# Kernel tuning notes

Measured on AMD Instinct MI355X. Metric: run time of the kernel, lower is better.

The kernel has to match this reference:

```python
import jax, jax.numpy as jnp
import numpy as np

BIG = jnp.float32(9e15)


def _normalize(sim, mask):
    # min/max are taken over positions where mask == 0 (faithful to the torch code)
    mn = jnp.min(jnp.where(mask == 0.0, sim, BIG), axis=-1, keepdims=True)
    mx = jnp.max(jnp.where(mask == 0.0, sim, -BIG), axis=-1, keepdims=True)
    return (sim - mn) / (mx - mn)


def setup_inputs() -> dict:
    key = jax.random.key(0)
    k1, k2 = jax.random.split(key)
    B, M = 4096, 8192
    return {
        "similarity_matrix": jax.random.normal(k1, (B, B), dtype=jnp.float32),
        "memory_bank_matrix": jax.random.normal(k2, (B, M), dtype=jnp.float32),
        "num_neighbors": 32,
        "temperature": jnp.ones((), dtype=jnp.float32),
    }


def reference(similarity_matrix, memory_bank_matrix, num_neighbors, temperature):
    sim = similarity_matrix
    B = sim.shape[0]
    eye = jnp.eye(B, dtype=sim.dtype)

    # --- neighbor masks via top-k over off-diagonal similarities ---
    sim_noself = jnp.where(eye == 0.0, sim, -BIG)
    _, topk_idx = jax.lax.top_k(sim_noself, num_neighbors)       # [B, k]
    rows = jnp.broadcast_to(jnp.arange(B)[:, None], topk_idx.shape)
    neighbor_mask = jnp.zeros((B, B), dtype=sim.dtype).at[rows, topk_idx].set(1.0)
    extended_mask = eye.at[rows, topk_idx].set(1.0)

    # --- centrality from memory bank ---
    centrality = jnp.mean(memory_bank_matrix, axis=-1)           # [B]
    cent_exp = jnp.broadcast_to(centrality[None, :], (B, B))

    norm_sim = _normalize(sim, extended_mask)
    norm_cent = _normalize(cent_exp, extended_mask)

    adjusted = jnp.where(neighbor_mask == 1.0, norm_sim - norm_cent, -BIG)

    # --- positive weights ---
    pw = jax.nn.softmax(adjusted * temperature, axis=-1)
    pw = jnp.where(neighbor_mask == 1.0, pw, 0.0)
    pw = jnp.where(eye == 1.0, 1.0, pw)  # fill_diagonal_(1.0)

    # --- masked log-softmax loss ---
    masked_sim = jnp.where(extended_mask == 1.0, sim, -BIG)
    logp = jax.nn.log_softmax(masked_sim, axis=-1) * pw
    per_row = -jnp.sum(logp, axis=-1) / jnp.sum(pw, axis=-1)
    return jnp.mean(per_row)
```

## Files before the change

### kernel.cpp

```cpp
#include <hip/hip_runtime.h>
#include <cmath>


#define CAP 256
#define MAXIT 40

__device__ inline float wave_max_f(float x) {
#pragma unroll
    for (int off = 32; off > 0; off >>= 1) x = fmaxf(x, __shfl_xor(x, off, 64));
    return x;
}
__device__ inline float wave_min_f(float x) {
#pragma unroll
    for (int off = 32; off > 0; off >>= 1) x = fminf(x, __shfl_xor(x, off, 64));
    return x;
}
__device__ inline float wave_sum_f(float x) {
#pragma unroll
    for (int off = 32; off > 0; off >>= 1) x += __shfl_xor(x, off, 64);
    return x;
}
__device__ inline unsigned int wave_min_u32(unsigned int x) {
#pragma unroll
    for (int off = 32; off > 0; off >>= 1) {
        unsigned int o = (unsigned int)__shfl_xor((int)x, off, 64);
        x = (o < x) ? o : x;
    }
    return x;
}

__device__ inline unsigned int f_to_key(float f) {
    unsigned int u = __float_as_uint(f);
    return u ^ ((u & 0x80000000u) ? 0xFFFFFFFFu : 0x80000000u);
}
__device__ inline float key_to_f(unsigned int key) {
    unsigned int u = key ^ ((key & 0x80000000u) ? 0x80000000u : 0xFFFFFFFFu);
    return __uint_as_float(u);
}

__global__ __launch_bounds__(256)
void cent_kernel(const float* __restrict__ mem, float* __restrict__ cent, int M) {
    __shared__ float s[4];
    const int row = blockIdx.x;
    const float4* p = (const float4*)(mem + (size_t)row * M);
    const int n4 = M >> 2;
    float acc = 0.0f;
    int i = threadIdx.x;
    for (; i + 1792 < n4; i += 2048) {
        float4 q0 = p[i], q1 = p[i + 256], q2 = p[i + 512], q3 = p[i + 768];
        float4 q4 = p[i + 1024], q5 = p[i + 1280], q6 = p[i + 1536], q7 = p[i + 1792];
        acc += ((q0.x + q0.y) + (q0.z + q0.w)) + ((q1.x + q1.y) + (q1.z + q1.w))
             + ((q2.x + q2.y) + (q2.z + q2.w)) + ((q3.x + q3.y) + (q3.z + q3.w))
             + ((q4.x + q4.y) + (q4.z + q4.w)) + ((q5.x + q5.y) + (q5.z + q5.w))
             + ((q6.x + q6.y) + (q6.z + q6.w)) + ((q7.x + q7.y) + (q7.z + q7.w));
    }
    for (; i < n4; i += 256) {
        float4 q = p[i];
        acc += (q.x + q.y) + (q.z + q.w);
    }
    acc = wave_sum_f(acc);
    const int lane = threadIdx.x & 63, wid = threadIdx.x >> 6;
    if (lane == 0) s[wid] = acc;
    __syncthreads();
    if (threadIdx.x == 0) cent[row] = (s[0] + s[1] + s[2] + s[3]) / (float)M;
}

__global__ __launch_bounds__(256)
void row_loss_kernel(const float* __restrict__ sim,
                     const float* __restrict__ cent,
                     const int* __restrict__ knn,
                     const float* __restrict__ temp_p,
                     float* __restrict__ per_row, int B) {
    __shared__ __align__(16) unsigned long long cand[CAP];
    __shared__ unsigned long long s_sel[64];
    __shared__ unsigned long long s_p33;
    __shared__ unsigned int s_kmin[4];
    __shared__ float s_cmin[4], s_cmax[4];
    __shared__ unsigned int s_cnt;
    __shared__ float s_diag;

    const int row = blockIdx.x, tid = threadIdx.x;
    const int lane = tid & 63, wid = tid >> 6;
    const int   k    = knn[0];
    const float temp = temp_p[0];

    unsigned int keys[16];
    unsigned int kmin = 0xFFFFFFFFu;
    const float4* rp = (const float4*)(sim + (size_t)row * B);
#pragma unroll
    for (int c = 0; c < 4; ++c) {
        float4 q = rp[c * 256 + tid];
        float t[4] = {q.x, q.y, q.z, q.w};
#pragma unroll
        for (int m = 0; m < 4; ++m) {
            const int j = c * 1024 + tid * 4 + m;
            unsigned int key = f_to_key(t[m]);
            if (j == row) { s_diag = t[m]; key = 0u; }
            else if (key < kmin) kmin = key;
            keys[c * 4 + m] = key;
        }
    }
    { unsigned int w = wave_min_u32(kmin); if (lane == 0) s_kmin[wid] = w; }
    if (tid == 0) { s_cnt = 0; s_p33 = ((unsigned long long)1u) << 32; }

    unsigned int keyT = f_to_key(2.0f), loK = 0u, hiK = 0xFFFFFFFFu, cnt = 0;
    const unsigned int need = (unsigned int)k + 1u;
    float cmin, cmax;
    const float4* cp = (const float4*)cent;
    for (int it = 0; it < MAXIT; ++it) {
        cmin = INFINITY; cmax = -INFINITY;
        __syncthreads();
#pragma unroll
        for (int c = 0; c < 4; ++c) {
            float4 q = cp[c * 256 + tid];
            float t[4] = {q.x, q.y, q.z, q.w};
#pragma unroll
            for (int m = 0; m < 4; ++m) {
                const unsigned int key = keys[c * 4 + m];
                if (key == 0u) continue;
                if (key > keyT) {
                    const unsigned int pos = atomicAdd(&s_cnt, 1u);
                    if (pos < CAP)
                        cand[pos] = ((unsigned long long)key << 32) |
                                    (unsigned long long)(0xFFFFFFFFu -
                                        (unsigned int)(c * 1024 + tid * 4 + m));
                } else {
                    cmin = fminf(cmin, t[m]);
                    cmax = fmaxf(cmax, t[m]);
                }
            }
        }
        { float a = wave_min_f(cmin), b = wave_max_f(cmax);
          if (lane == 0) { s_cmin[wid] = a; s_cmax[wid] = b; } }
        __syncthreads();
        cnt = s_cnt;
        if (cnt >= need && cnt <= CAP) break;
        if (cnt < need) { hiK = keyT; keyT = loK + ((keyT - loK) >> 1); }
        else            { loK = keyT; keyT = keyT + ((hiK - keyT) >> 1); }
        if (tid == 0) s_cnt = 0;
    }
    if (wid != 0) return;

    {
        const unsigned int n = min(cnt, (unsigned int)CAP);
        const unsigned int p0 = lane, p1 = lane + 64u, p2 = lane + 128u, p3 = lane + 192u;
        unsigned long long own0 = 0ull, own1 = 0ull, own2 = 0ull, own3 = 0ull;
        if (p0 < n) own0 = cand[p0];
        if (p1 < n) own1 = cand[p1];
        if (p2 < n) own2 = cand[p2];
        if (p3 < n) own3 = cand[p3];
        unsigned int r0 = 0, r1 = 0, r2 = 0, r3 = 0;
        const ulonglong2* c2 = (const ulonglong2*)cand;
        const unsigned int np = n >> 1;
        for (unsigned int o = 0; o < np; ++o) {
            ulonglong2 pr = c2[o];
            r0 += (pr.x > own0) ? 1u : 0u; r0 += (pr.y > own0) ? 1u : 0u;
            r1 += (pr.x > own1) ? 1u : 0u; r1 += (pr.y > own1) ? 1u : 0u;
            r2 += (pr.x > own2) ? 1u : 0u; r2 += (pr.y > own2) ? 1u : 0u;
            r3 += (pr.x > own3) ? 1u : 0u; r3 += (pr.y > own3) ? 1u : 0u;
        }
        if (n & 1u) {
            unsigned long long x = cand[n - 1u];
            r0 += (x > own0) ? 1u : 0u; r1 += (x > own1) ? 1u : 0u;
            r2 += (x > own2) ? 1u : 0u; r3 += (x > own3) ? 1u : 0u;
        }
        float cmin2 = INFINITY, cmax2 = -INFINITY;
        const unsigned int uk = (unsigned int)k;
#define HANDLE(P, OWN, R)                                                     \
        if ((P) < n) {                                                        \
            if ((R) < uk) s_sel[R] = (OWN);                                   \
            else if ((R) == uk) s_p33 = (OWN);                                \
            if ((R) >= uk) {                                                  \
                const int jj = (int)(0xFFFFFFFFu - (unsigned int)(OWN));      \
                const float cv = cent[jj];                                    \
                cmin2 = fminf(cmin2, cv);                                     \
                cmax2 = fmaxf(cmax2, cv);                                     \
            }                                                                 \
        }
        HANDLE(p0, own0, r0)
        HANDLE(p1, own1, r1)
        HANDLE(p2, own2, r2)
        HANDLE(p3, own3, r3)
#undef HANDLE
        __builtin_amdgcn_wave_barrier();
        cmin2 = wave_min_f(cmin2);
        cmax2 = wave_max_f(cmax2);
        const float mn_c = fminf(cmin2,
            fminf(fminf(s_cmin[0], s_cmin[1]), fminf(s_cmin[2], s_cmin[3])));
        const float mx_c = fmaxf(cmax2,
            fmaxf(fmaxf(s_cmax[0], s_cmax[1]), fmaxf(s_cmax[2], s_cmax[3])));
        const unsigned int kminb =
            min(min(s_kmin[0], s_kmin[1]), min(s_kmin[2], s_kmin[3]));
        const float mn_s = key_to_f(kminb);
        const float mx_s = key_to_f((unsigned int)(s_p33 >> 32));

        const float sdiag = s_diag;
        const bool  act = (lane < k);
        const unsigned long long sel = act ? s_sel[lane] : 0ull;
        const float sj = act ? key_to_f((unsigned int)(sel >> 32)) : -INFINITY;
        const int   j  = act ? (int)(0xFFFFFFFFu - (unsigned int)sel) : 0;
        const float cj = cent[j];

        float a = -INFINITY;
        if (act) {
            const float ns = (sj - mn_s) / (mx_s - mn_s);
            const float nc = (cj - mn_c) / (mx_c - mn_c);
            a = (ns - nc) * temp;
        }
        const float am   = wave_max_f(a);
        const float e    = act ? expf(a - am) : 0.0f;
        const float esum = wave_sum_f(e);
        const float pw   = e / esum;

        const float m2  = fmaxf(wave_max_f(sj), sdiag);
        const float ex  = act ? expf(sj - m2) : 0.0f;
        const float lse = m2 + logf(wave_sum_f(ex) + expf(sdiag - m2));

        const float num = wave_sum_f(act ? pw * (sj - lse) : 0.0f) + (sdiag - lse);
        const float den = 1.0f + wave_sum_f(pw);
        if (lane == 0) per_row[row] = -num / den;
    }
}

__global__ __launch_bounds__(256)
void reduce_kernel(const float* __restrict__ per_row, float* __restrict__ out, int B) {
    __shared__ float s[4];
    float acc = 0.0f;
    const float4* p = (const float4*)per_row;
    const int n4 = B >> 2;
    for (int i = threadIdx.x; i < n4; i += 256) {
        float4 q = p[i];
        acc += (q.x + q.y) + (q.z + q.w);
    }
    acc = wave_sum_f(acc);
    const int lane = threadIdx.x & 63, wid = threadIdx.x >> 6;
    if (lane == 0) s[wid] = acc;
    __syncthreads();
    if (threadIdx.x == 0) out[0] = (s[0] + s[1] + s[2] + s[3]) / (float)B;
}

extern "C" void kernel_launch(void* const* d_in, const int* in_sizes, int n_in,
                              void* d_out, int out_size, void* d_ws, size_t ws_size,
                              hipStream_t stream) {
    const float* sim  = (const float*)d_in[0];
    const float* mem  = (const float*)d_in[1];
    const int*   knn  = (const int*)d_in[2];
    const float* temp = (const float*)d_in[3];
    float* out     = (float*)d_out;
    float* cent    = (float*)d_ws;
    float* per_row = (float*)d_ws + 4096;

    const int B = (int)(std::sqrt((double)in_sizes[0]) + 0.5);
    const int M = in_sizes[1] / B;

    cent_kernel<<<B, 256, 0, stream>>>(mem, cent, M);
    row_loss_kernel<<<B, 256, 0, stream>>>(sim, cent, knn, temp, per_row, B);
    reduce_kernel<<<1, 256, 0, stream>>>(per_row, out, B);
}
```

Baseline: 56.31 us.

## Merge centrality and top-k selection into one launch, defer centrality min/max to finale

Centrality averaging and per-row top-k threshold search now run in one interleaved grid, so the memory-bank read and the similarity read overlap instead of running back to back. The centrality min/max over non-neighbour columns no longer sits inside the bisection loop. It moves to a new finale kernel that builds a per-row bitmask of neighbours and scans the centrality vector once. The final mean is folded into the finale through a last-block atomic counter. The costs are workspace round-trips for the selected candidates and headers, plus reliance on the counter being reset in pass 1.

```diff
diff --git a/kernel.cpp b/kernel.cpp
--- a/kernel.cpp
+++ b/kernel.cpp
@@ -39,50 +39,52 @@
 }
 
 __global__ __launch_bounds__(256)
-void cent_kernel(const float* __restrict__ mem, float* __restrict__ cent, int M) {
-    __shared__ float s[4];
-    const int row = blockIdx.x;
-    const float4* p = (const float4*)(mem + (size_t)row * M);
-    const int n4 = M >> 2;
-    float acc = 0.0f;
-    int i = threadIdx.x;
-    for (; i + 1792 < n4; i += 2048) {
-        float4 q0 = p[i], q1 = p[i + 256], q2 = p[i + 512], q3 = p[i + 768];
-        float4 q4 = p[i + 1024], q5 = p[i + 1280], q6 = p[i + 1536], q7 = p[i + 1792];
-        acc += ((q0.x + q0.y) + (q0.z + q0.w)) + ((q1.x + q1.y) + (q1.z + q1.w))
-             + ((q2.x + q2.y) + (q2.z + q2.w)) + ((q3.x + q3.y) + (q3.z + q3.w))
-             + ((q4.x + q4.y) + (q4.z + q4.w)) + ((q5.x + q5.y) + (q5.z + q5.w))
-             + ((q6.x + q6.y) + (q6.z + q6.w)) + ((q7.x + q7.y) + (q7.z + q7.w));
-    }
-    for (; i < n4; i += 256) {
-        float4 q = p[i];
-        acc += (q.x + q.y) + (q.z + q.w);
-    }
-    acc = wave_sum_f(acc);
-    const int lane = threadIdx.x & 63, wid = threadIdx.x >> 6;
-    if (lane == 0) s[wid] = acc;
-    __syncthreads();
-    if (threadIdx.x == 0) cent[row] = (s[0] + s[1] + s[2] + s[3]) / (float)M;
-}
-
-__global__ __launch_bounds__(256)
-void row_loss_kernel(const float* __restrict__ sim,
-                     const float* __restrict__ cent,
-                     const int* __restrict__ knn,
-                     const float* __restrict__ temp_p,
-                     float* __restrict__ per_row, int B) {
+void pass1_kernel(const float* __restrict__ sim,
+                  const float* __restrict__ mem,
+                  const int* __restrict__ knn,
+                  float* __restrict__ cent,
+                  uint4* __restrict__ hdr,
+                  unsigned long long* __restrict__ selbuf,
+                  unsigned int* __restrict__ ctr,
+                  int B, int M) {
     __shared__ __align__(16) unsigned long long cand[CAP];
-    __shared__ unsigned long long s_sel[64];
     __shared__ unsigned long long s_p33;
     __shared__ unsigned int s_kmin[4];
-    __shared__ float s_cmin[4], s_cmax[4];
     __shared__ unsigned int s_cnt;
     __shared__ float s_diag;
-
-    const int row = blockIdx.x, tid = threadIdx.x;
+    __shared__ float s_red[4];
+
+    const int bid = blockIdx.x, tid = threadIdx.x;
     const int lane = tid & 63, wid = tid >> 6;
-    const int   k    = knn[0];
-    const float temp = temp_p[0];
+    const int g = bid >> 3;
+    const int row = (g >> 1) * 8 + (bid & 7);
+
+    if ((g & 1) == 0) {
+        if (bid == 0 && tid == 0) ctr[0] = 0u;
+        const float4* p = (const float4*)(mem + (size_t)row * M);
+        const int n4 = M >> 2;
+        float acc = 0.0f;
+        int i = tid;
+        for (; i + 1792 < n4; i += 2048) {
+            float4 q0 = p[i], q1 = p[i + 256], q2 = p[i + 512], q3 = p[i + 768];
+            float4 q4 = p[i + 1024], q5 = p[i + 1280], q6 = p[i + 1536], q7 = p[i + 1792];
+            acc += ((q0.x + q0.y) + (q0.z + q0.w)) + ((q1.x + q1.y) + (q1.z + q1.w))
+                 + ((q2.x + q2.y) + (q2.z + q2.w)) + ((q3.x + q3.y) + (q3.z + q3.w))
+                 + ((q4.x + q4.y) + (q4.z + q4.w)) + ((q5.x + q5.y) + (q5.z + q5.w))
+                 + ((q6.x + q6.y) + (q6.z + q6.w)) + ((q7.x + q7.y) + (q7.z + q7.w));
+        }
+        for (; i < n4; i += 256) {
+            float4 q = p[i];
+            acc += (q.x + q.y) + (q.z + q.w);
+        }
+        acc = wave_sum_f(acc);
+        if (lane == 0) s_red[wid] = acc;
+        __syncthreads();
+        if (tid == 0) cent[row] = (s_red[0] + s_red[1] + s_red[2] + s_red[3]) / (float)M;
+        return;
+    }
+
+    const int k = knn[0];
 
     unsigned int keys[16];
     unsigned int kmin = 0xFFFFFFFFu;
@@ -105,33 +107,22 @@
 
     unsigned int keyT = f_to_key(2.0f), loK = 0u, hiK = 0xFFFFFFFFu, cnt = 0;
     const unsigned int need = (unsigned int)k + 1u;
-    float cmin, cmax;
-    const float4* cp = (const float4*)cent;
     for (int it = 0; it < MAXIT; ++it) {
-        cmin = INFINITY; cmax = -INFINITY;
         __syncthreads();
 #pragma unroll
         for (int c = 0; c < 4; ++c) {
-            float4 q = cp[c * 256 + tid];
-            float t[4] = {q.x, q.y, q.z, q.w};
 #pragma unroll
             for (int m = 0; m < 4; ++m) {
                 const unsigned int key = keys[c * 4 + m];
-                if (key == 0u) continue;
                 if (key > keyT) {
                     const unsigned int pos = atomicAdd(&s_cnt, 1u);
                     if (pos < CAP)
                         cand[pos] = ((unsigned long long)key << 32) |
                                     (unsigned long long)(0xFFFFFFFFu -
                                         (unsigned int)(c * 1024 + tid * 4 + m));
-                } else {
-                    cmin = fminf(cmin, t[m]);
-                    cmax = fmaxf(cmax, t[m]);
                 }
             }
         }
-        { float a = wave_min_f(cmin), b = wave_max_f(cmax);
-          if (lane == 0) { s_cmin[wid] = a; s_cmax[wid] = b; } }
         __syncthreads();
         cnt = s_cnt;
         if (cnt >= need && cnt <= CAP) break;
@@ -164,18 +155,11 @@
             r0 += (x > own0) ? 1u : 0u; r1 += (x > own1) ? 1u : 0u;
             r2 += (x > own2) ? 1u : 0u; r3 += (x > own3) ? 1u : 0u;
         }
-        float cmin2 = INFINITY, cmax2 = -INFINITY;
         const unsigned int uk = (unsigned int)k;
 #define HANDLE(P, OWN, R)                                                     \
         if ((P) < n) {                                                        \
-            if ((R) < uk) s_sel[R] = (OWN);                                   \
+            if ((R) < uk) selbuf[(size_t)row * 64 + (R)] = (OWN);             \
             else if ((R) == uk) s_p33 = (OWN);                                \
-            if ((R) >= uk) {                                                  \
-                const int jj = (int)(0xFFFFFFFFu - (unsigned int)(OWN));      \
-                const float cv = cent[jj];                                    \
-                cmin2 = fminf(cmin2, cv);                                     \
-                cmax2 = fmaxf(cmax2, cv);                                     \
-            }                                                                 \
         }
         HANDLE(p0, own0, r0)
         HANDLE(p1, own1, r1)
@@ -183,60 +167,110 @@
         HANDLE(p3, own3, r3)
 #undef HANDLE
         __builtin_amdgcn_wave_barrier();
-        cmin2 = wave_min_f(cmin2);
-        cmax2 = wave_max_f(cmax2);
-        const float mn_c = fminf(cmin2,
-            fminf(fminf(s_cmin[0], s_cmin[1]), fminf(s_cmin[2], s_cmin[3])));
-        const float mx_c = fmaxf(cmax2,
-            fmaxf(fmaxf(s_cmax[0], s_cmax[1]), fmaxf(s_cmax[2], s_cmax[3])));
-        const unsigned int kminb =
-            min(min(s_kmin[0], s_kmin[1]), min(s_kmin[2], s_kmin[3]));
-        const float mn_s = key_to_f(kminb);
-        const float mx_s = key_to_f((unsigned int)(s_p33 >> 32));
-
-        const float sdiag = s_diag;
-        const bool  act = (lane < k);
-        const unsigned long long sel = act ? s_sel[lane] : 0ull;
-        const float sj = act ? key_to_f((unsigned int)(sel >> 32)) : -INFINITY;
-        const int   j  = act ? (int)(0xFFFFFFFFu - (unsigned int)sel) : 0;
-        const float cj = cent[j];
-
-        float a = -INFINITY;
-        if (act) {
-            const float ns = (sj - mn_s) / (mx_s - mn_s);
-            const float nc = (cj - mn_c) / (mx_c - mn_c);
-            a = (ns - nc) * temp;
-        }
-        const float am   = wave_max_f(a);
-        const float e    = act ? expf(a - am) : 0.0f;
-        const float esum = wave_sum_f(e);
-        const float pw   = e / esum;
-
-        const float m2  = fmaxf(wave_max_f(sj), sdiag);
-        const float ex  = act ? expf(sj - m2) : 0.0f;
-        const float lse = m2 + logf(wave_sum_f(ex) + expf(sdiag - m2));
-
-        const float num = wave_sum_f(act ? pw * (sj - lse) : 0.0f) + (sdiag - lse);
-        const float den = 1.0f + wave_sum_f(pw);
-        if (lane == 0) per_row[row] = -num / den;
+        if (lane == 0) {
+            const unsigned int kminb =
+                min(min(s_kmin[0], s_kmin[1]), min(s_kmin[2], s_kmin[3]));
+            uint4 h;
+            h.x = kminb;
+            h.y = (unsigned int)(s_p33 >> 32);
+            h.z = __float_as_uint(s_diag);
+            h.w = cnt;
+            hdr[row] = h;
+        }
     }
 }
 
 __global__ __launch_bounds__(256)
-void reduce_kernel(const float* __restrict__ per_row, float* __restrict__ out, int B) {
-    __shared__ float s[4];
-    float acc = 0.0f;
-    const float4* p = (const float4*)per_row;
-    const int n4 = B >> 2;
-    for (int i = threadIdx.x; i < n4; i += 256) {
-        float4 q = p[i];
-        acc += (q.x + q.y) + (q.z + q.w);
-    }
-    acc = wave_sum_f(acc);
-    const int lane = threadIdx.x & 63, wid = threadIdx.x >> 6;
-    if (lane == 0) s[wid] = acc;
+void finale_kernel(const float* __restrict__ cent,
+                   const uint4* __restrict__ hdr,
+                   const unsigned long long* __restrict__ selbuf,
+                   const int* __restrict__ knn,
+                   const float* __restrict__ temp_p,
+                   float* __restrict__ per_row,
+                   unsigned int* __restrict__ ctr,
+                   float* __restrict__ out, int B) {
+    __shared__ unsigned int bm[4 * 128];
+    __shared__ float s_red[4];
+    __shared__ int s_last;
+
+    const int tid = threadIdx.x, lane = tid & 63, wid = tid >> 6;
+    const int row = (blockIdx.x << 2) + wid;
+    const int k = knn[0];
+    const float temp = temp_p[0];
+
+    const uint4 h = hdr[row];
+    const float mn_s = key_to_f(h.x);
+    const float mx_s = key_to_f(h.y);
+    const float sdiag = __uint_as_float(h.z);
+
+    const bool act = (lane < k);
+    const unsigned long long sel = act ? selbuf[(size_t)row * 64 + lane] : 0ull;
+    const float sj = act ? key_to_f((unsigned int)(sel >> 32)) : -INFINITY;
+    const int   j  = act ? (int)(0xFFFFFFFFu - (unsigned int)sel) : 0;
+    const float cj = cent[j];
+
+    unsigned int* mybm = &bm[wid * 128];
+    mybm[lane * 2] = 0u; mybm[lane * 2 + 1] = 0u;
+    __builtin_amdgcn_wave_barrier();
+    if (act) atomicOr(&mybm[((unsigned int)j) >> 5], 1u << (j & 31));
+    if (lane == 0) atomicOr(&mybm[((unsigned int)row) >> 5], 1u << (row & 31));
+    __builtin_amdgcn_wave_barrier();
+
+    float cmin = INFINITY, cmax = -INFINITY;
+    const float4* c4 = (const float4*)cent;
+#pragma unroll
+    for (int it = 0; it < 16; ++it) {
+        const float4 v = c4[it * 64 + lane];
+        const unsigned int w = mybm[it * 8 + (lane >> 3)];
+        const unsigned int nib = w >> ((lane & 7) * 4);
+        if (!(nib & 1u)) { cmin = fminf(cmin, v.x); cmax = fmaxf(cmax, v.x); }
+        if (!(nib & 2u)) { cmin = fminf(cmin, v.y); cmax = fmaxf(cmax, v.y); }
+        if (!(nib & 4u)) { cmin = fminf(cmin, v.z); cmax = fmaxf(cmax, v.z); }
+        if (!(nib & 8u)) { cmin = fminf(cmin, v.w); cmax = fmaxf(cmax, v.w); }
+    }
+    const float mn_c = wave_min_f(cmin);
+    const float mx_c = wave_max_f(cmax);
+
+    float a = -INFINITY;
+    if (act) {
+        const float ns = (sj - mn_s) / (mx_s - mn_s);
+        const float nc = (cj - mn_c) / (mx_c - mn_c);
+        a = (ns - nc) * temp;
+    }
+    const float am   = wave_max_f(a);
+    const float e    = act ? expf(a - am) : 0.0f;
+    const float esum = wave_sum_f(e);
+    const float pw   = e / esum;
+
+    const float m2  = fmaxf(wave_max_f(sj), sdiag);
+    const float ex  = act ? expf(sj - m2) : 0.0f;
+    const float lse = m2 + logf(wave_sum_f(ex) + expf(sdiag - m2));
+
+    const float num = wave_sum_f(act ? pw * (sj - lse) : 0.0f) + (sdiag - lse);
+    const float den = 1.0f + wave_sum_f(pw);
+    if (lane == 0) per_row[row] = -num / den;
+
     __syncthreads();
-    if (threadIdx.x == 0) out[0] = (s[0] + s[1] + s[2] + s[3]) / (float)B;
+    if (tid == 0) {
+        __threadfence();
+        const unsigned int prev = atomicAdd(ctr, 1u);
+        s_last = (prev == (unsigned int)(gridDim.x - 1u)) ? 1 : 0;
+    }
+    __syncthreads();
+    if (s_last) {
+        __threadfence();
+        float acc = 0.0f;
+        const float4* p = (const float4*)per_row;
+        const int n4 = B >> 2;
+        for (int i = tid; i < n4; i += 256) {
+            float4 q = p[i];
+            acc += (q.x + q.y) + (q.z + q.w);
+        }
+        acc = wave_sum_f(acc);
+        if (lane == 0) s_red[wid] = acc;
+        __syncthreads();
+        if (tid == 0) out[0] = (s_red[0] + s_red[1] + s_red[2] + s_red[3]) / (float)B;
+    }
 }
 
 extern "C" void kernel_launch(void* const* d_in, const int* in_sizes, int n_in,
@@ -246,14 +280,18 @@
     const float* mem  = (const float*)d_in[1];
     const int*   knn  = (const int*)d_in[2];
     const float* temp = (const float*)d_in[3];
-    float* out     = (float*)d_out;
-    float* cent    = (float*)d_ws;
-    float* per_row = (float*)d_ws + 4096;
+    float* out = (float*)d_out;
+
+    char* ws = (char*)d_ws;
+    float*              cent    = (float*)ws;
+    float*              per_row = (float*)(ws + 16384);
+    unsigned int*       ctr     = (unsigned int*)(ws + 32768);
+    uint4*              hdr     = (uint4*)(ws + 49152);
+    unsigned long long* selbuf  = (unsigned long long*)(ws + 114688);
 
     const int B = (int)(std::sqrt((double)in_sizes[0]) + 0.5);
     const int M = in_sizes[1] / B;
 
-    cent_kernel<<<B, 256, 0, stream>>>(mem, cent, M);
-    row_loss_kernel<<<B, 256, 0, stream>>>(sim, cent, knn, temp, per_row, B);
-    reduce_kernel<<<1, 256, 0, stream>>>(per_row, out, B);
-}
+    pass1_kernel<<<2 * B, 256, 0, stream>>>(sim, mem, knn, cent, hdr, selbuf, ctr, B, M);
+    finale_kernel<<<B / 4, 256, 0, stream>>>(cent, hdr, selbuf, knn, temp, per_row, ctr, out, B);
+}
```

Measured after the change: 74.37 us. 32.1% more time.
